# Kernel optimization log

Hardware: AMD Instinct MI355X
Metric: run time of the kernel (lower is better)

Reference implementation:

```python
import jax, jax.numpy as jnp
import numpy as np

# HUSM region -> channel mapping (19 channels, 4 disjoint regions)
REGIONS = [
    [0, 1, 5, 8, 9, 10, 14],    # frontal
    [2, 11, 17],                # central
    [3, 12, 18],                # parietal
    [4, 6, 7, 13, 15, 16],      # occipital
]
N_CHAN = 19
N_REG = 4
_region_id = np.empty(N_CHAN, dtype=np.int32)
for r, chans in enumerate(REGIONS):
    for c in chans:
        _region_id[c] = r
REGION_ID = jnp.array(_region_id)
REGION_COUNTS = jnp.array([len(r) for r in REGIONS], dtype=jnp.float32)

N_HEADS, D_K, D_V, D_MODEL, D_FF = 8, 32, 32, 256, 1024
EPS = 1e-5


def layernorm(x):
    # default nn.LayerNorm: gamma=1, beta=0 (layer re-created each forward)
    mu = jnp.mean(x, axis=-1, keepdims=True)
    var = jnp.var(x, axis=-1, keepdims=True)
    return (x - mu) * jax.lax.rsqrt(var + EPS)


def mha(q_in, k_in, v_in, wq, wk, wv, wo):
    # q_in: [B, S, D]
    B, S, _ = q_in.shape
    Q = jnp.einsum('bsd,dhk->bhsk', q_in, wq.reshape(D_MODEL, N_HEADS, D_K))
    K = jnp.einsum('bsd,dhk->bhsk', k_in, wk.reshape(D_MODEL, N_HEADS, D_K))
    V = jnp.einsum('bsd,dhv->bhsv', v_in, wv.reshape(D_MODEL, N_HEADS, D_V))
    scores = jnp.einsum('bhqk,bhsk->bhqs', Q, K) / jnp.sqrt(jnp.float32(D_K))
    attn = jax.nn.softmax(scores, axis=-1)
    ctx = jnp.einsum('bhqs,bhsv->bqhv', attn, V).reshape(B, S, N_HEADS * D_V)
    return layernorm(ctx @ wo + q_in)


def setup_inputs() -> dict:
    key = jax.random.key(0)
    ks = jax.random.split(key, 12)
    B = 4096
    sc = 1.0 / np.sqrt(D_MODEL)
    inp = {
        'x': jax.random.normal(ks[0], (B, N_CHAN, D_MODEL), dtype=jnp.float32),
        'rsa_wq': jax.random.normal(ks[1], (D_MODEL, D_MODEL), dtype=jnp.float32) * sc,
        'rsa_wk': jax.random.normal(ks[2], (D_MODEL, D_MODEL), dtype=jnp.float32) * sc,
        'rsa_wv': jax.random.normal(ks[3], (D_MODEL, D_MODEL), dtype=jnp.float32) * sc,
        'rsa_wo': jax.random.normal(ks[4], (D_MODEL, D_MODEL), dtype=jnp.float32) * sc,
        'lsa_wq': jax.random.normal(ks[5], (D_MODEL, D_MODEL), dtype=jnp.float32) * sc,
        'lsa_wk': jax.random.normal(ks[6], (D_MODEL, D_MODEL), dtype=jnp.float32) * sc,
        'lsa_wv': jax.random.normal(ks[7], (D_MODEL, D_MODEL), dtype=jnp.float32) * sc,
        'lsa_wo': jax.random.normal(ks[8], (D_MODEL, D_MODEL), dtype=jnp.float32) * sc,
        'ffn_w1': jax.random.normal(ks[9], (D_MODEL, D_FF), dtype=jnp.float32) * sc,
        'ffn_w2': jax.random.normal(ks[10], (D_FF, D_MODEL), dtype=jnp.float32) * (1.0 / np.sqrt(D_FF)),
    }
    return inp


def reference(x, rsa_wq, rsa_wk, rsa_wv, rsa_wo,
              lsa_wq, lsa_wk, lsa_wv, lsa_wo, ffn_w1, ffn_w2):
    # --- region gather + avgpool: mean of channels per region -> [B, 4, D]
    fe_sum = jax.ops.segment_sum(jnp.swapaxes(x, 0, 1), REGION_ID,
                                 num_segments=N_REG)          # [4, B, D]
    fe_region = jnp.swapaxes(fe_sum, 0, 1) / REGION_COUNTS[None, :, None]
    # --- tiny 4-token region self-attention
    refined = mha(fe_region, fe_region, fe_region,
                  rsa_wq, rsa_wk, rsa_wv, rsa_wo)             # [B, 4, D]
    # --- scatter-add refined region feature back to its channels
    x = x + refined[:, REGION_ID, :]                          # [B, 19, D]
    # --- full-channel MHA + FFN
    fused = mha(x, x, x, lsa_wq, lsa_wk, lsa_wv, lsa_wo)
    ffn = jax.nn.relu(fused @ ffn_w1) @ ffn_w2
    return layernorm(ffn + fused)
```

## Files before the change

### kernel.cpp

```cpp
#include <hip/hip_runtime.h>
#include <stdint.h>
#include <stddef.h>


#define DEVINL __device__ __forceinline__

typedef __attribute__((ext_vector_type(8))) short short8;
typedef __attribute__((ext_vector_type(4))) float floatx4;
typedef __attribute__((ext_vector_type(8))) unsigned short ushort8;
typedef __attribute__((ext_vector_type(4))) unsigned short ushort4v;

DEVINL float bf2f(unsigned short u){
  union { unsigned int i; float f; } x; x.i = ((unsigned int)u) << 16; return x.f;
}
DEVINL unsigned short f2bf(float f){
  union { float f; unsigned int i; } x; x.f = f;
  unsigned int r = x.i + 0x7fffu + ((x.i >> 16) & 1u);
  return (unsigned short)(r >> 16);
}

typedef __attribute__((address_space(1))) void gvoid_t;
typedef __attribute__((address_space(3))) void lvoid_t;
DEVINL void gload_lds16(const void* g, void* l){
  __builtin_amdgcn_global_load_lds((gvoid_t*)g, (lvoid_t*)l, 16, 0, 0);
}

__global__ __launch_bounds__(256) void wprep_all(
    const float* __restrict__ rq, const float* __restrict__ rk,
    const float* __restrict__ rv, const float* __restrict__ ro,
    const float* __restrict__ lq, const float* __restrict__ lk,
    const float* __restrict__ lv, const float* __restrict__ lo,
    const float* __restrict__ w1, const float* __restrict__ w2,
    unsigned short* __restrict__ wt)
{
  int idx = blockIdx.x * 256 + threadIdx.x;
  const float* W; unsigned short* D; int N, r;
  const int K = (idx < 786432) ? 256 : 1024;
  if (idx < 524288){
    int wsel = idx >> 16; r = idx & 65535; N = 256; D = wt + wsel * 65536;
    switch (wsel){
      case 0: W = rq; break; case 1: W = rk; break; case 2: W = rv; break; case 3: W = ro; break;
      case 4: W = lq; break; case 5: W = lk; break; case 6: W = lv; break; default: W = lo; break;
    }
  } else if (idx < 786432){
    r = idx - 524288; N = 1024; D = wt + 524288; W = w1;
  } else {
    r = idx - 786432; N = 256; D = wt + 786432; W = w2;
  }
  int k = r / N, n = r - k * N;
  D[(size_t)n * K + k] = f2bf(W[r]);
}

__global__ __launch_bounds__(256) void pool_kernel(const float* __restrict__ x,
                                                   unsigned short* __restrict__ fe)
{
  const int b = blockIdx.x, d = threadIdx.x;
  const float* xb = x + (size_t)b * 4864 + d;
  float s0 = xb[0*256]+xb[1*256]+xb[5*256]+xb[8*256]+xb[9*256]+xb[10*256]+xb[14*256];
  float s1 = xb[2*256]+xb[11*256]+xb[17*256];
  float s2 = xb[3*256]+xb[12*256]+xb[18*256];
  float s3 = xb[4*256]+xb[6*256]+xb[7*256]+xb[13*256]+xb[15*256]+xb[16*256];
  unsigned short* fb = fe + (size_t)b * 1024 + d;
  fb[0]   = f2bf(s0 * (1.f/7.f));
  fb[256] = f2bf(s1 * (1.f/3.f));
  fb[512] = f2bf(s2 * (1.f/3.f));
  fb[768] = f2bf(s3 * (1.f/6.f));
}

template<int RELU>
__global__ __launch_bounds__(256, 2)
void gemm_kernel(const unsigned short* __restrict__ A,
                 const unsigned short* __restrict__ Bt,
                 unsigned short* __restrict__ C, int M, int N, int K)
{
  __shared__ __align__(1024) unsigned short lds[2][2][8192];
  const int tid  = threadIdx.x;
  const int wave = tid >> 6, lane = tid & 63;
  const int wm = wave >> 1, wn = wave & 1;
  const int rowA0 = blockIdx.x * 128;
  const int rowB0 = blockIdx.y * 128;
  const int stg_row = lane >> 3;
  const int stg_kb  = (((lane & 7) ^ (lane >> 3)) << 4);

  floatx4 acc[4][4];
  #pragma unroll
  for (int i = 0; i < 4; ++i)
    #pragma unroll
    for (int j = 0; j < 4; ++j) acc[i][j] = (floatx4){0.f, 0.f, 0.f, 0.f};

  const int nk = K >> 6;
  int cur = 0;
  #pragma unroll
  for (int s = 0; s < 4; ++s){
    int chunk = wave * 4 + s;
    int r = chunk * 8 + stg_row;
    gload_lds16((const char*)(A  + (size_t)(rowA0 + r) * K) + stg_kb,
                (char*)(&lds[0][0][0]) + chunk * 1024);
    gload_lds16((const char*)(Bt + (size_t)(rowB0 + r) * K) + stg_kb,
                (char*)(&lds[0][1][0]) + chunk * 1024);
  }
  __syncthreads();

  for (int kt = 0; kt < nk; ++kt){
    if (kt + 1 < nk){
      const int kbase = (kt + 1) << 7;
      #pragma unroll
      for (int s = 0; s < 4; ++s){
        int chunk = wave * 4 + s;
        int r = chunk * 8 + stg_row;
        gload_lds16((const char*)(A  + (size_t)(rowA0 + r) * K) + kbase + stg_kb,
                    (char*)(&lds[cur ^ 1][0][0]) + chunk * 1024);
        gload_lds16((const char*)(Bt + (size_t)(rowB0 + r) * K) + kbase + stg_kb,
                    (char*)(&lds[cur ^ 1][1][0]) + chunk * 1024);
      }
    }
    const char* As = (const char*)(&lds[cur][0][0]);
    const char* Bs = (const char*)(&lds[cur][1][0]);
    #pragma unroll
    for (int kk = 0; kk < 2; ++kk){
      short8 a[4], b[4];
      #pragma unroll
      for (int i = 0; i < 4; ++i){
        int row = wm * 64 + i * 16 + (lane & 15);
        int kb  = (kk * 64 + ((lane >> 4) << 4)) ^ ((row & 7) << 4);
        a[i] = *(const short8*)(As + row * 128 + kb);
      }
      #pragma unroll
      for (int j = 0; j < 4; ++j){
        int row = wn * 64 + j * 16 + (lane & 15);
        int kb  = (kk * 64 + ((lane >> 4) << 4)) ^ ((row & 7) << 4);
        b[j] = *(const short8*)(Bs + row * 128 + kb);
      }
      #pragma unroll
      for (int i = 0; i < 4; ++i)
        #pragma unroll
        for (int j = 0; j < 4; ++j)
          acc[i][j] = __builtin_amdgcn_mfma_f32_16x16x32_bf16(a[i], b[j], acc[i][j], 0, 0, 0);
    }
    __syncthreads();
    cur ^= 1;
  }

  const int cr = (lane >> 4) << 2;
  const int cc = lane & 15;
  #pragma unroll
  for (int i = 0; i < 4; ++i){
    #pragma unroll
    for (int j = 0; j < 4; ++j){
      int r0 = rowA0 + wm * 64 + i * 16 + cr;
      int c0 = rowB0 + wn * 64 + j * 16 + cc;
      #pragma unroll
      for (int r = 0; r < 4; ++r){
        float v = acc[i][j][r];
        if (RELU) v = fmaxf(v, 0.f);
        C[(size_t)(r0 + r) * N + c0] = f2bf(v);
      }
    }
  }
}

__global__ __launch_bounds__(256) void attn4_kernel(
    const unsigned short* __restrict__ Q, const unsigned short* __restrict__ K,
    const unsigned short* __restrict__ V, unsigned short* __restrict__ ctx)
{
  const int t = threadIdx.x;
  const int lb = t >> 5, u = t & 31, h = u >> 2, q = u & 3;
  const size_t b = (size_t)blockIdx.x * 8 + lb;
  const size_t base = b * 1024 + h * 32;

  float qf[32];
  {
    const ushort8* qp = (const ushort8*)(Q + base + q * 256);
    #pragma unroll
    for (int g = 0; g < 4; ++g){
      ushort8 v = qp[g];
      #pragma unroll
      for (int e = 0; e < 8; ++e) qf[g * 8 + e] = bf2f(v[e]);
    }
  }
  float sc[4];
  #pragma unroll
  for (int s = 0; s < 4; ++s){
    const ushort8* kp = (const ushort8*)(K + base + s * 256);
    float a0 = 0, a1 = 0, a2 = 0, a3 = 0;
    #pragma unroll
    for (int g = 0; g < 4; ++g){
      ushort8 v = kp[g];
      a0 += qf[g*8+0]*bf2f(v[0]); a1 += qf[g*8+1]*bf2f(v[1]);
      a2 += qf[g*8+2]*bf2f(v[2]); a3 += qf[g*8+3]*bf2f(v[3]);
      a0 += qf[g*8+4]*bf2f(v[4]); a1 += qf[g*8+5]*bf2f(v[5]);
      a2 += qf[g*8+6]*bf2f(v[6]); a3 += qf[g*8+7]*bf2f(v[7]);
    }
    sc[s] = ((a0 + a1) + (a2 + a3)) * 0.17677669529663687f;
  }
  float m = fmaxf(fmaxf(sc[0], sc[1]), fmaxf(sc[2], sc[3]));
  float sum = 0.f;
  #pragma unroll
  for (int s = 0; s < 4; ++s){ sc[s] = __expf(sc[s] - m); sum += sc[s]; }
  float inv = 1.f / sum;

  float o[32];
  #pragma unroll
  for (int d = 0; d < 32; ++d) o[d] = 0.f;
  #pragma unroll
  for (int s = 0; s < 4; ++s){
    float p = sc[s] * inv;
    const ushort8* vp = (const ushort8*)(V + base + s * 256);
    #pragma unroll
    for (int g = 0; g < 4; ++g){
      ushort8 v = vp[g];
      #pragma unroll
      for (int e = 0; e < 8; ++e) o[g * 8 + e] += p * bf2f(v[e]);
    }
  }
  unsigned short* cp = ctx + base + q * 256;
  #pragma unroll
  for (int g = 0; g < 4; ++g){
    ushort8 w;
    #pragma unroll
    for (int e = 0; e < 8; ++e) w[e] = f2bf(o[g * 8 + e]);
    ((ushort8*)cp)[g] = w;
  }
}

__global__ __launch_bounds__(256) void rsa_finish_kernel(
    const float* __restrict__ x, const unsigned short* __restrict__ o4,
    const unsigned short* __restrict__ fe, unsigned short* __restrict__ x2)
{
  const int b = blockIdx.x, d = threadIdx.x;
  const int wave = d >> 6, lane = d & 63;
  float v[4];
  #pragma unroll
  for (int r = 0; r < 4; ++r){
    size_t idx = (size_t)b * 1024 + r * 256 + d;
    v[r] = bf2f(o4[idx]) + bf2f(fe[idx]);
  }
  __shared__ float red[2][4][4];
  #pragma unroll
  for (int r = 0; r < 4; ++r){
    float s = v[r], ss = v[r] * v[r];
    #pragma unroll
    for (int off = 32; off; off >>= 1){ s += __shfl_xor(s, off); ss += __shfl_xor(ss, off); }
    if (lane == 0){ red[0][wave][r] = s; red[1][wave][r] = ss; }
  }
  __syncthreads();
  #pragma unroll
  for (int r = 0; r < 4; ++r){
    float S  = red[0][0][r] + red[0][1][r] + red[0][2][r] + red[0][3][r];
    float SS = red[1][0][r] + red[1][1][r] + red[1][2][r] + red[1][3][r];
    float mu = S * (1.f / 256.f);
    float var = SS * (1.f / 256.f) - mu * mu;
    v[r] = (v[r] - mu) * rsqrtf(var + 1e-5f);
  }
  const float* xb = x + (size_t)b * 4864 + d;
  unsigned short* xo = x2 + (size_t)b * 4864 + d;
  const int rid[19] = {0,0,1,2,3,0,3,3,0,0,0,1,2,3,0,3,3,1,2};
  #pragma unroll
  for (int c = 0; c < 19; ++c) xo[c * 256] = f2bf(xb[c * 256] + v[rid[c]]);
}

__global__ __launch_bounds__(256) void attn19_kernel(
    const unsigned short* __restrict__ Q, const unsigned short* __restrict__ K,
    const unsigned short* __restrict__ V, unsigned short* __restrict__ ctx)
{
  __shared__ float Kl[4864];
  __shared__ float Vl[4864];
  const size_t b = blockIdx.x;
  const unsigned short* Kb = K + b * 4864;
  const unsigned short* Vb = V + b * 4864;
  for (int i = threadIdx.x; i < 4864; i += 256){ Kl[i] = bf2f(Kb[i]); Vl[i] = bf2f(Vb[i]); }
  __syncthreads();
  const int t = threadIdx.x;
  if (t >= 152) return;
  const int h = t / 19, qq = t - h * 19;

  float qf[32];
  {
    const ushort8* qp = (const ushort8*)(Q + b * 4864 + qq * 256 + h * 32);
    #pragma unroll
    for (int g = 0; g < 4; ++g){
      ushort8 v = qp[g];
      #pragma unroll
      for (int e = 0; e < 8; ++e) qf[g * 8 + e] = bf2f(v[e]);
    }
  }
  float p[19];
  float m = -1e30f;
  #pragma unroll
  for (int s = 0; s < 19; ++s){
    const float* kr = &Kl[s * 256 + h * 32];
    float a0 = 0, a1 = 0, a2 = 0, a3 = 0;
    #pragma unroll
    for (int d = 0; d < 32; d += 4){
      a0 += qf[d+0] * kr[d+0]; a1 += qf[d+1] * kr[d+1];
      a2 += qf[d+2] * kr[d+2]; a3 += qf[d+3] * kr[d+3];
    }
    p[s] = ((a0 + a1) + (a2 + a3)) * 0.17677669529663687f;
    m = fmaxf(m, p[s]);
  }
  float sum = 0.f;
  #pragma unroll
  for (int s = 0; s < 19; ++s){ p[s] = __expf(p[s] - m); sum += p[s]; }
  float inv = 1.f / sum;

  float o[32];
  #pragma unroll
  for (int d = 0; d < 32; ++d) o[d] = 0.f;
  #pragma unroll
  for (int s = 0; s < 19; ++s){
    float ps = p[s] * inv;
    const float* vr = &Vl[s * 256 + h * 32];
    #pragma unroll
    for (int d = 0; d < 32; ++d) o[d] += ps * vr[d];
  }
  unsigned short* cp = ctx + b * 4864 + qq * 256 + h * 32;
  #pragma unroll
  for (int g = 0; g < 4; ++g){
    ushort8 w;
    #pragma unroll
    for (int e = 0; e < 8; ++e) w[e] = f2bf(o[g * 8 + e]);
    ((ushort8*)cp)[g] = w;
  }
}

template<int BF16OUT>
__global__ __launch_bounds__(256) void addln_kernel(
    const unsigned short* __restrict__ a, const unsigned short* __restrict__ b,
    void* __restrict__ outp)
{
  const int row = blockIdx.x * 4 + (threadIdx.x >> 6);
  const int lane = threadIdx.x & 63;
  const size_t base = (size_t)row * 256;
  ushort4v av = *(const ushort4v*)(a + base + lane * 4);
  ushort4v bv = *(const ushort4v*)(b + base + lane * 4);
  float v[4];
  #pragma unroll
  for (int i = 0; i < 4; ++i) v[i] = bf2f(av[i]) + bf2f(bv[i]);
  float s = (v[0] + v[1]) + (v[2] + v[3]);
  float ss = (v[0]*v[0] + v[1]*v[1]) + (v[2]*v[2] + v[3]*v[3]);
  #pragma unroll
  for (int off = 32; off; off >>= 1){ s += __shfl_xor(s, off); ss += __shfl_xor(ss, off); }
  float mu = s * (1.f / 256.f);
  float var = ss * (1.f / 256.f) - mu * mu;
  float rs = rsqrtf(var + 1e-5f);
  if (BF16OUT){
    ushort4v w;
    #pragma unroll
    for (int i = 0; i < 4; ++i) w[i] = f2bf((v[i] - mu) * rs);
    *(ushort4v*)((unsigned short*)outp + base + lane * 4) = w;
  } else {
    floatx4 w;
    #pragma unroll
    for (int i = 0; i < 4; ++i) w[i] = (v[i] - mu) * rs;
    *(floatx4*)((float*)outp + base + lane * 4) = w;
  }
}

extern "C" void kernel_launch(void* const* d_in, const int* in_sizes, int n_in,
                              void* d_out, int out_size, void* d_ws, size_t ws_size,
                              hipStream_t stream)
{
  (void)n_in; (void)out_size;
  const float* x  = (const float*)d_in[0];
  const float* rq = (const float*)d_in[1];
  const float* rk = (const float*)d_in[2];
  const float* rv = (const float*)d_in[3];
  const float* ro = (const float*)d_in[4];
  const float* lq = (const float*)d_in[5];
  const float* lk = (const float*)d_in[6];
  const float* lv = (const float*)d_in[7];
  const float* lo = (const float*)d_in[8];
  const float* w1 = (const float*)d_in[9];
  const float* w2 = (const float*)d_in[10];

  const int B = in_sizes[0] / 4864;
  const int M4  = B * 4;
  const int M19 = B * 19;
  const size_t MB = 1ull << 20;
  if (ws_size < 240 * MB) return;

  char* ws = (char*)d_ws;
  unsigned short* WT    = (unsigned short*)(ws);
  unsigned short* FE    = (unsigned short*)(ws + 2   * MB);
  unsigned short* Q4    = (unsigned short*)(ws + 10  * MB);
  unsigned short* K4    = (unsigned short*)(ws + 18  * MB);
  unsigned short* V4    = (unsigned short*)(ws + 26  * MB);
  unsigned short* CTX4  = (unsigned short*)(ws + 34  * MB);
  unsigned short* O4    = (unsigned short*)(ws + 42  * MB);
  unsigned short* X2    = (unsigned short*)(ws + 50  * MB);
  unsigned short* Q19   = (unsigned short*)(ws + 88  * MB);
  unsigned short* K19   = (unsigned short*)(ws + 126 * MB);
  unsigned short* V19   = (unsigned short*)(ws + 164 * MB);
  unsigned short* CTX19 = (unsigned short*)(ws + 202 * MB);
  unsigned short* O19   = (unsigned short*)(ws + 88  * MB);
  unsigned short* FUSED = (unsigned short*)(ws + 126 * MB);
  unsigned short* H     = (unsigned short*)(ws + 164 * MB);
  unsigned short* F2    = (unsigned short*)(ws + 50  * MB);
  float* out = (float*)d_out;

  wprep_all<<<4096, 256, 0, stream>>>(rq, rk, rv, ro, lq, lk, lv, lo, w1, w2, WT);
  pool_kernel<<<B, 256, 0, stream>>>(x, FE);
  gemm_kernel<0><<<dim3(M4/128, 2), 256, 0, stream>>>(FE, WT + 0*65536, Q4, M4, 256, 256);
  gemm_kernel<0><<<dim3(M4/128, 2), 256, 0, stream>>>(FE, WT + 1*65536, K4, M4, 256, 256);
  gemm_kernel<0><<<dim3(M4/128, 2), 256, 0, stream>>>(FE, WT + 2*65536, V4, M4, 256, 256);
  attn4_kernel<<<B/8, 256, 0, stream>>>(Q4, K4, V4, CTX4);
  gemm_kernel<0><<<dim3(M4/128, 2), 256, 0, stream>>>(CTX4, WT + 3*65536, O4, M4, 256, 256);
  rsa_finish_kernel<<<B, 256, 0, stream>>>(x, O4, FE, X2);
  gemm_kernel<0><<<dim3(M19/128, 2), 256, 0, stream>>>(X2, WT + 4*65536, Q19, M19, 256, 256);
  gemm_kernel<0><<<dim3(M19/128, 2), 256, 0, stream>>>(X2, WT + 5*65536, K19, M19, 256, 256);
  gemm_kernel<0><<<dim3(M19/128, 2), 256, 0, stream>>>(X2, WT + 6*65536, V19, M19, 256, 256);
  attn19_kernel<<<B, 256, 0, stream>>>(Q19, K19, V19, CTX19);
  gemm_kernel<0><<<dim3(M19/128, 2), 256, 0, stream>>>(CTX19, WT + 7*65536, O19, M19, 256, 256);
  addln_kernel<1><<<M19/4, 256, 0, stream>>>(O19, X2, FUSED);
  const int MH = M19 / 2;
  for (int hf = 0; hf < 2; ++hf){
    const unsigned short* Ain = FUSED + (size_t)hf * MH * 256;
    unsigned short* F2h = F2 + (size_t)hf * MH * 256;
    gemm_kernel<1><<<dim3(MH/128, 8), 256, 0, stream>>>(Ain, WT + 524288, H, MH, 1024, 256);
    gemm_kernel<0><<<dim3(MH/128, 2), 256, 0, stream>>>(H, WT + 786432, F2h, MH, 256, 1024);
  }
  addln_kernel<0><<<M19/4, 256, 0, stream>>>(F2, FUSED, out);
}
```

Measured before the change: 428.9 us.

## Fuse QKV projections into one GEMM and fold residual+LayerNorm into GEMM epilogue

Merges the separate Q, K and V projection GEMMs into a single GEMM with N=768 against contiguous transposed weights, and changes the attention kernels to read the interleaved QKV layout. Adds a 512-thread GEMM kernel that covers the full 256-wide output row per block, so residual add and LayerNorm run in its epilogue. This removes the standalone add+LN kernels and their intermediate writes and reads. Attn19 now keeps K/V in bf16 in padded LDS. The cost is the LN GEMM running one block per CU with fewer blocks in the grid, and a larger output tile per block.

Measured after the change: 476.9 us. 11.2% more time.

```diff
diff --git a/kernel.cpp b/kernel.cpp
--- a/kernel.cpp
+++ b/kernel.cpp
@@ -159,18 +159,140 @@
   }
 }
 
+template<int OUTF32>
+__global__ __launch_bounds__(512, 1)
+void gemm_ln_kernel(const unsigned short* __restrict__ A,
+                    const unsigned short* __restrict__ Bt,
+                    const unsigned short* __restrict__ Res,
+                    void* __restrict__ Out, int M, int K)
+{
+  __shared__ __align__(1024) char lds[2][49152];
+  __shared__ float red_s[4][128], red_q[4][128];
+  __shared__ float tot_mu[128], tot_rs[128];
+  const int tid  = threadIdx.x;
+  const int wave = tid >> 6, lane = tid & 63;
+  const int wm = wave >> 2, wn = wave & 3;
+  const int rowA0 = blockIdx.x * 128;
+  const int stg_row = lane >> 3;
+  const int stg_kb  = (((lane & 7) ^ (lane >> 3)) << 4);
+
+  floatx4 acc[4][4];
+  #pragma unroll
+  for (int i = 0; i < 4; ++i)
+    #pragma unroll
+    for (int j = 0; j < 4; ++j) acc[i][j] = (floatx4){0.f, 0.f, 0.f, 0.f};
+
+  const int nk = K >> 6;
+  int cur = 0;
+  #pragma unroll
+  for (int s = 0; s < 6; ++s){
+    int chunk = wave * 6 + s;
+    const unsigned short* src;
+    if (chunk < 16) src = A  + (size_t)(rowA0 + chunk * 8 + stg_row) * K;
+    else            src = Bt + (size_t)((chunk - 16) * 8 + stg_row) * K;
+    gload_lds16((const char*)src + stg_kb, &lds[0][0] + chunk * 1024);
+  }
+  __syncthreads();
+
+  for (int kt = 0; kt < nk; ++kt){
+    if (kt + 1 < nk){
+      const int kbase = (kt + 1) << 7;
+      #pragma unroll
+      for (int s = 0; s < 6; ++s){
+        int chunk = wave * 6 + s;
+        const unsigned short* src;
+        if (chunk < 16) src = A  + (size_t)(rowA0 + chunk * 8 + stg_row) * K;
+        else            src = Bt + (size_t)((chunk - 16) * 8 + stg_row) * K;
+        gload_lds16((const char*)src + kbase + stg_kb, &lds[cur ^ 1][0] + chunk * 1024);
+      }
+    }
+    const char* As = &lds[cur][0];
+    const char* Bs = &lds[cur][0] + 16384;
+    #pragma unroll
+    for (int kk = 0; kk < 2; ++kk){
+      short8 a[4], b[4];
+      #pragma unroll
+      for (int i = 0; i < 4; ++i){
+        int row = wm * 64 + i * 16 + (lane & 15);
+        int kb  = (kk * 64 + ((lane >> 4) << 4)) ^ ((row & 7) << 4);
+        a[i] = *(const short8*)(As + row * 128 + kb);
+      }
+      #pragma unroll
+      for (int j = 0; j < 4; ++j){
+        int row = wn * 64 + j * 16 + (lane & 15);
+        int kb  = (kk * 64 + ((lane >> 4) << 4)) ^ ((row & 7) << 4);
+        b[j] = *(const short8*)(Bs + row * 128 + kb);
+      }
+      #pragma unroll
+      for (int i = 0; i < 4; ++i)
+        #pragma unroll
+        for (int j = 0; j < 4; ++j)
+          acc[i][j] = __builtin_amdgcn_mfma_f32_16x16x32_bf16(a[i], b[j], acc[i][j], 0, 0, 0);
+    }
+    __syncthreads();
+    cur ^= 1;
+  }
+
+  const int g  = lane >> 4;
+  const int cl = lane & 15;
+  #pragma unroll
+  for (int i = 0; i < 4; ++i){
+    #pragma unroll
+    for (int r = 0; r < 4; ++r){
+      const int rowl = wm * 64 + i * 16 + g * 4 + r;
+      float s = 0.f, q = 0.f;
+      #pragma unroll
+      for (int j = 0; j < 4; ++j){
+        float v = acc[i][j][r] +
+                  bf2f(Res[(size_t)(rowA0 + rowl) * 256 + wn * 64 + j * 16 + cl]);
+        acc[i][j][r] = v;
+        s += v; q += v * v;
+      }
+      #pragma unroll
+      for (int off = 1; off < 16; off <<= 1){
+        s += __shfl_xor(s, off); q += __shfl_xor(q, off);
+      }
+      if (cl == 0){ red_s[wn][rowl] = s; red_q[wn][rowl] = q; }
+    }
+  }
+  __syncthreads();
+  if (tid < 128){
+    float S = red_s[0][tid] + red_s[1][tid] + red_s[2][tid] + red_s[3][tid];
+    float Q = red_q[0][tid] + red_q[1][tid] + red_q[2][tid] + red_q[3][tid];
+    float mu = S * (1.f / 256.f);
+    float var = Q * (1.f / 256.f) - mu * mu;
+    tot_mu[tid] = mu;
+    tot_rs[tid] = rsqrtf(var + 1e-5f);
+  }
+  __syncthreads();
+  #pragma unroll
+  for (int i = 0; i < 4; ++i){
+    #pragma unroll
+    for (int r = 0; r < 4; ++r){
+      const int rowl = wm * 64 + i * 16 + g * 4 + r;
+      const float mu = tot_mu[rowl], rs = tot_rs[rowl];
+      #pragma unroll
+      for (int j = 0; j < 4; ++j){
+        float w = (acc[i][j][r] - mu) * rs;
+        size_t idx = (size_t)(rowA0 + rowl) * 256 + wn * 64 + j * 16 + cl;
+        if (OUTF32) ((float*)Out)[idx] = w;
+        else        ((unsigned short*)Out)[idx] = f2bf(w);
+      }
+    }
+  }
+}
+
 __global__ __launch_bounds__(256) void attn4_kernel(
-    const unsigned short* __restrict__ Q, const unsigned short* __restrict__ K,
-    const unsigned short* __restrict__ V, unsigned short* __restrict__ ctx)
+    const unsigned short* __restrict__ QKV, unsigned short* __restrict__ ctx)
 {
   const int t = threadIdx.x;
   const int lb = t >> 5, u = t & 31, h = u >> 2, q = u & 3;
   const size_t b = (size_t)blockIdx.x * 8 + lb;
-  const size_t base = b * 1024 + h * 32;
+  const unsigned short* tb = QKV + b * 4 * 768;
 
   float qf[32];
   {
-    const ushort8* qp = (const ushort8*)(Q + base + q * 256);
+    const ushort8* qp = (const ushort8*)(tb + (size_t)q * 768 + h * 32);
     #pragma unroll
     for (int g = 0; g < 4; ++g){
       ushort8 v = qp[g];
@@ -181,7 +303,7 @@
   float sc[4];
   #pragma unroll
   for (int s = 0; s < 4; ++s){
-    const ushort8* kp = (const ushort8*)(K + base + s * 256);
+    const ushort8* kp = (const ushort8*)(tb + (size_t)s * 768 + 256 + h * 32);
     float a0 = 0, a1 = 0, a2 = 0, a3 = 0;
     #pragma unroll
     for (int g = 0; g < 4; ++g){
@@ -205,7 +327,7 @@
   #pragma unroll
   for (int s = 0; s < 4; ++s){
     float p = sc[s] * inv;
-    const ushort8* vp = (const ushort8*)(V + base + s * 256);
+    const ushort8* vp = (const ushort8*)(tb + (size_t)s * 768 + 512 + h * 32);
     #pragma unroll
     for (int g = 0; g < 4; ++g){
       ushort8 v = vp[g];
@@ -213,7 +335,7 @@
       for (int e = 0; e < 8; ++e) o[g * 8 + e] += p * bf2f(v[e]);
     }
   }
-  unsigned short* cp = ctx + base + q * 256;
+  unsigned short* cp = ctx + (b * 4 + q) * 256 + h * 32;
   #pragma unroll
   for (int g = 0; g < 4; ++g){
     ushort8 w;
@@ -223,60 +345,47 @@
   }
 }
 
-__global__ __launch_bounds__(256) void rsa_finish_kernel(
-    const float* __restrict__ x, const unsigned short* __restrict__ o4,
-    const unsigned short* __restrict__ fe, unsigned short* __restrict__ x2)
+__global__ __launch_bounds__(256) void scatter_kernel(
+    const float* __restrict__ x, const unsigned short* __restrict__ ref,
+    unsigned short* __restrict__ x2)
 {
   const int b = blockIdx.x, d = threadIdx.x;
-  const int wave = d >> 6, lane = d & 63;
-  float v[4];
-  #pragma unroll
-  for (int r = 0; r < 4; ++r){
-    size_t idx = (size_t)b * 1024 + r * 256 + d;
-    v[r] = bf2f(o4[idx]) + bf2f(fe[idx]);
-  }
-  __shared__ float red[2][4][4];
-  #pragma unroll
-  for (int r = 0; r < 4; ++r){
-    float s = v[r], ss = v[r] * v[r];
-    #pragma unroll
-    for (int off = 32; off; off >>= 1){ s += __shfl_xor(s, off); ss += __shfl_xor(ss, off); }
-    if (lane == 0){ red[0][wave][r] = s; red[1][wave][r] = ss; }
-  }
-  __syncthreads();
-  #pragma unroll
-  for (int r = 0; r < 4; ++r){
-    float S  = red[0][0][r] + red[0][1][r] + red[0][2][r] + red[0][3][r];
-    float SS = red[1][0][r] + red[1][1][r] + red[1][2][r] + red[1][3][r];
-    float mu = S * (1.f / 256.f);
-    float var = SS * (1.f / 256.f) - mu * mu;
-    v[r] = (v[r] - mu) * rsqrtf(var + 1e-5f);
-  }
+  float rv[4];
+  #pragma unroll
+  for (int r = 0; r < 4; ++r) rv[r] = bf2f(ref[(size_t)b * 1024 + r * 256 + d]);
   const float* xb = x + (size_t)b * 4864 + d;
   unsigned short* xo = x2 + (size_t)b * 4864 + d;
   const int rid[19] = {0,0,1,2,3,0,3,3,0,0,0,1,2,3,0,3,3,1,2};
   #pragma unroll
-  for (int c = 0; c < 19; ++c) xo[c * 256] = f2bf(xb[c * 256] + v[rid[c]]);
+  for (int c = 0; c < 19; ++c) xo[c * 256] = f2bf(xb[c * 256] + rv[rid[c]]);
 }
 
 __global__ __launch_bounds__(256) void attn19_kernel(
-    const unsigned short* __restrict__ Q, const unsigned short* __restrict__ K,
-    const unsigned short* __restrict__ V, unsigned short* __restrict__ ctx)
-{
-  __shared__ float Kl[4864];
-  __shared__ float Vl[4864];
+    const unsigned short* __restrict__ QKV, unsigned short* __restrict__ ctx)
+{
+  __shared__ unsigned short Kl[19][264];
+  __shared__ unsigned short Vl[19][264];
   const size_t b = blockIdx.x;
-  const unsigned short* Kb = K + b * 4864;
-  const unsigned short* Vb = V + b * 4864;
-  for (int i = threadIdx.x; i < 4864; i += 256){ Kl[i] = bf2f(Kb[i]); Vl[i] = bf2f(Vb[i]); }
+  const unsigned short* base = QKV + b * 19 * 768;
+
+  for (int v = threadIdx.x; v < 1216; v += 256){
+    int m = (v >= 608);
+    int i = v - (m ? 608 : 0);
+    int s = i >> 5;
+    int c = (i & 31) << 3;
+    ushort8 w = *(const ushort8*)(base + (size_t)s * 768 + 256 + (m << 8) + c);
+    if (m) *(ushort8*)(&Vl[s][c]) = w;
+    else   *(ushort8*)(&Kl[s][c]) = w;
+  }
   __syncthreads();
+
   const int t = threadIdx.x;
   if (t >= 152) return;
   const int h = t / 19, qq = t - h * 19;
 
   float qf[32];
   {
-    const ushort8* qp = (const ushort8*)(Q + b * 4864 + qq * 256 + h * 32);
+    const ushort8* qp = (const ushort8*)(base + (size_t)qq * 768 + h * 32);
     #pragma unroll
     for (int g = 0; g < 4; ++g){
       ushort8 v = qp[g];
@@ -288,12 +397,13 @@
   float m = -1e30f;
   #pragma unroll
   for (int s = 0; s < 19; ++s){
-    const float* kr = &Kl[s * 256 + h * 32];
+    const unsigned short* kr = &Kl[s][h * 32];
     float a0 = 0, a1 = 0, a2 = 0, a3 = 0;
     #pragma unroll
-    for (int d = 0; d < 32; d += 4){
-      a0 += qf[d+0] * kr[d+0]; a1 += qf[d+1] * kr[d+1];
-      a2 += qf[d+2] * kr[d+2]; a3 += qf[d+3] * kr[d+3];
+    for (int g = 0; g < 8; ++g){
+      ushort4v kv = *(const ushort4v*)(kr + g * 4);
+      a0 += qf[g*4+0] * bf2f(kv[0]); a1 += qf[g*4+1] * bf2f(kv[1]);
+      a2 += qf[g*4+2] * bf2f(kv[2]); a3 += qf[g*4+3] * bf2f(kv[3]);
     }
     p[s] = ((a0 + a1) + (a2 + a3)) * 0.17677669529663687f;
     m = fmaxf(m, p[s]);
@@ -309,50 +419,21 @@
   #pragma unroll
   for (int s = 0; s < 19; ++s){
     float ps = p[s] * inv;
-    const float* vr = &Vl[s * 256 + h * 32];
-    #pragma unroll
-    for (int d = 0; d < 32; ++d) o[d] += ps * vr[d];
-  }
-  unsigned short* cp = ctx + b * 4864 + qq * 256 + h * 32;
+    const unsigned short* vr = &Vl[s][h * 32];
+    #pragma unroll
+    for (int g = 0; g < 8; ++g){
+      ushort4v vv = *(const ushort4v*)(vr + g * 4);
+      o[g*4+0] += ps * bf2f(vv[0]); o[g*4+1] += ps * bf2f(vv[1]);
+      o[g*4+2] += ps * bf2f(vv[2]); o[g*4+3] += ps * bf2f(vv[3]);
+    }
+  }
+  unsigned short* cp = ctx + (b * 19 + qq) * 256 + h * 32;
   #pragma unroll
   for (int g = 0; g < 4; ++g){
     ushort8 w;
     #pragma unroll
     for (int e = 0; e < 8; ++e) w[e] = f2bf(o[g * 8 + e]);
     ((ushort8*)cp)[g] = w;
-  }
-}
-
-template<int BF16OUT>
-__global__ __launch_bounds__(256) void addln_kernel(
-    const unsigned short* __restrict__ a, const unsigned short* __restrict__ b,
-    void* __restrict__ outp)
-{
-  const int row = blockIdx.x * 4 + (threadIdx.x >> 6);
-  const int lane = threadIdx.x & 63;
-  const size_t base = (size_t)row * 256;
-  ushort4v av = *(const ushort4v*)(a + base + lane * 4);
-  ushort4v bv = *(const ushort4v*)(b + base + lane * 4);
-  float v[4];
-  #pragma unroll
-  for (int i = 0; i < 4; ++i) v[i] = bf2f(av[i]) + bf2f(bv[i]);
-  float s = (v[0] + v[1]) + (v[2] + v[3]);
-  float ss = (v[0]*v[0] + v[1]*v[1]) + (v[2]*v[2] + v[3]*v[3]);
-  #pragma unroll
-  for (int off = 32; off; off >>= 1){ s += __shfl_xor(s, off); ss += __shfl_xor(ss, off); }
-  float mu = s * (1.f / 256.f);
-  float var = ss * (1.f / 256.f) - mu * mu;
-  float rs = rsqrtf(var + 1e-5f);
-  if (BF16OUT){
-    ushort4v w;
-    #pragma unroll
-    for (int i = 0; i < 4; ++i) w[i] = f2bf((v[i] - mu) * rs);
-    *(ushort4v*)((unsigned short*)outp + base + lane * 4) = w;
-  } else {
-    floatx4 w;
-    #pragma unroll
-    for (int i = 0; i < 4; ++i) w[i] = (v[i] - mu) * rs;
-    *(floatx4*)((float*)outp + base + lane * 4) = w;
   }
 }
 
@@ -376,48 +457,36 @@
   const int B = in_sizes[0] / 4864;
   const int M4  = B * 4;
   const int M19 = B * 19;
+  const int MH  = M19 / 2;
   const size_t MB = 1ull << 20;
   if (ws_size < 240 * MB) return;
 
   char* ws = (char*)d_ws;
   unsigned short* WT    = (unsigned short*)(ws);
   unsigned short* FE    = (unsigned short*)(ws + 2   * MB);
-  unsigned short* Q4    = (unsigned short*)(ws + 10  * MB);
-  unsigned short* K4    = (unsigned short*)(ws + 18  * MB);
-  unsigned short* V4    = (unsigned short*)(ws + 26  * MB);
+  unsigned short* QKV4  = (unsigned short*)(ws + 10  * MB);
   unsigned short* CTX4  = (unsigned short*)(ws + 34  * MB);
-  unsigned short* O4    = (unsigned short*)(ws + 42  * MB);
+  unsigned short* REF   = (unsigned short*)(ws + 42  * MB);
   unsigned short* X2    = (unsigned short*)(ws + 50  * MB);
-  unsigned short* Q19   = (unsigned short*)(ws + 88  * MB);
-  unsigned short* K19   = (unsigned short*)(ws + 126 * MB);
-  unsigned short* V19   = (unsigned short*)(ws + 164 * MB);
+  unsigned short* QKV19 = (unsigned short*)(ws + 88  * MB);
   unsigned short* CTX19 = (unsigned short*)(ws + 202 * MB);
-  unsigned short* O19   = (unsigned short*)(ws + 88  * MB);
-  unsigned short* FUSED = (unsigned short*)(ws + 126 * MB);
-  unsigned short* H     = (unsigned short*)(ws + 164 * MB);
-  unsigned short* F2    = (unsigned short*)(ws + 50  * MB);
+  unsigned short* FUSED = (unsigned short*)(ws + 88  * MB);
+  unsigned short* H     = (unsigned short*)(ws + 126 * MB);
   float* out = (float*)d_out;
 
   wprep_all<<<4096, 256, 0, stream>>>(rq, rk, rv, ro, lq, lk, lv, lo, w1, w2, WT);
   pool_kernel<<<B, 256, 0, stream>>>(x, FE);
-  gemm_kernel<0><<<dim3(M4/128, 2), 256, 0, stream>>>(FE, WT + 0*65536, Q4, M4, 256, 256);
-  gemm_kernel<0><<<dim3(M4/128, 2), 256, 0, stream>>>(FE, WT + 1*65536, K4, M4, 256, 256);
-  gemm_kernel<0><<<dim3(M4/128, 2), 256, 0, stream>>>(FE, WT + 2*65536, V4, M4, 256, 256);
-  attn4_kernel<<<B/8, 256, 0, stream>>>(Q4, K4, V4, CTX4);
-  gemm_kernel<0><<<dim3(M4/128, 2), 256, 0, stream>>>(CTX4, WT + 3*65536, O4, M4, 256, 256);
-  rsa_finish_kernel<<<B, 256, 0, stream>>>(x, O4, FE, X2);
-  gemm_kernel<0><<<dim3(M19/128, 2), 256, 0, stream>>>(X2, WT + 4*65536, Q19, M19, 256, 256);
-  gemm_kernel<0><<<dim3(M19/128, 2), 256, 0, stream>>>(X2, WT + 5*65536, K19, M19, 256, 256);
-  gemm_kernel<0><<<dim3(M19/128, 2), 256, 0, stream>>>(X2, WT + 6*65536, V19, M19, 256, 256);
-  attn19_kernel<<<B, 256, 0, stream>>>(Q19, K19, V19, CTX19);
-  gemm_kernel<0><<<dim3(M19/128, 2), 256, 0, stream>>>(CTX19, WT + 7*65536, O19, M19, 256, 256);
-  addln_kernel<1><<<M19/4, 256, 0, stream>>>(O19, X2, FUSED);
-  const int MH = M19 / 2;
+  gemm_kernel<0><<<dim3(M4/128, 6), 256, 0, stream>>>(FE, WT, QKV4, M4, 768, 256);
+  attn4_kernel<<<B/8, 256, 0, stream>>>(QKV4, CTX4);
+  gemm_ln_kernel<0><<<M4/128, 512, 0, stream>>>(CTX4, WT + 3*65536, FE, REF, M4, 256);
+  scatter_kernel<<<B, 256, 0, stream>>>(x, REF, X2);
+  gemm_kernel<0><<<dim3(M19/128, 6), 256, 0, stream>>>(X2, WT + 4*65536, QKV19, M19, 768, 256);
+  attn19_kernel<<<B, 256, 0, stream>>>(QKV19, CTX19);
+  gemm_ln_kernel<0><<<M19/128, 512, 0, stream>>>(CTX19, WT + 7*65536, X2, FUSED, M19, 256);
   for (int hf = 0; hf < 2; ++hf){
-    const unsigned short* Ain = FUSED + (size_t)hf * MH * 256;
-    unsigned short* F2h = F2 + (size_t)hf * MH * 256;
-    gemm_kernel<1><<<dim3(MH/128, 8), 256, 0, stream>>>(Ain, WT + 524288, H, MH, 1024, 256);
-    gemm_kernel<0><<<dim3(MH/128, 2), 256, 0, stream>>>(H, WT + 786432, F2h, MH, 256, 1024);
-  }
-  addln_kernel<0><<<M19/4, 256, 0, stream>>>(F2, FUSED, out);
-}
+    const unsigned short* Fh = FUSED + (size_t)hf * MH * 256;
+    gemm_kernel<1><<<dim3(MH/128, 8), 256, 0, stream>>>(Fh, WT + 524288, H, MH, 1024, 256);
+    gemm_ln_kernel<1><<<MH/128, 512, 0, stream>>>(H, WT + 786432, Fh,
+                                                  out + (size_t)hf * MH * 256, MH, 1024);
+  }
+}
```
